# Optimization experiments

Hardware: AMD Instinct MI355X
Metric: run time of the kernel (lower is better)

The kernel has to match this reference:

```python
import jax, jax.numpy as jnp
import numpy as np

B, L, DK, DV, H, DKL, DVL, R = 64, 4096, 128, 128, 4, 64, 128, 128


def setup_inputs() -> dict:
    key = jax.random.key(0)
    ks = jax.random.split(key, 7)
    K = jax.random.normal(ks[0], (B, L, DK), dtype=jnp.float32)
    V = jax.random.normal(ks[1], (B, L, DV), dtype=jnp.float32)
    mask = jax.random.uniform(ks[2], (B, L)) < 0.25
    mask = mask.at[:, 0].set(False)
    # Learned parameters (Wq is zeros at init in the original; use small random
    # values so the softmax is non-degenerate for correctness testing)
    Wq = jax.random.normal(ks[3], (H, DKL), dtype=jnp.float32) * 0.02
    Wk = jax.random.normal(ks[4], (DK, H, DKL), dtype=jnp.float32) / np.sqrt(DK)
    Wv = jax.random.normal(ks[5], (DV, H, DVL), dtype=jnp.float32) / np.sqrt(DV)
    Wo = jax.random.normal(ks[6], (H, DVL, R), dtype=jnp.float32) / np.sqrt(H * DVL)
    return {"K": K, "V": V, "mask": mask, "Wq": Wq, "Wk": Wk, "Wv": Wv, "Wo": Wo}


def reference(K, V, mask, Wq, Wk, Wv, Wo):
    # scale = 1/sqrt(dim_q), dim_q == dim_k
    scale = 1.0 / jnp.sqrt(jnp.asarray(K.shape[-1], K.dtype))
    Kp = jnp.einsum('bld,dhk->blhk', K, Wk)          # (B, L, H, DKL)
    Vp = jnp.einsum('ble,ehv->blhv', V, Wv)          # (B, L, H, DVL)
    QK = jnp.einsum('hk,blhk->blh', Wq, Kp)          # (B, L, H)
    QK = jnp.where(mask[..., None], -jnp.inf, QK)    # mask over set axis L
    w = jax.nn.softmax(scale * QK, axis=-2)          # softmax over L (dim=-2)
    # nanmean over the set axis (masked positions contribute w=0; NaN entries,
    # if present in V, are skipped exactly as torch.nanmean does)
    QKV = jnp.nanmean(w[..., None] * Vp, axis=-3)    # (B, H, DVL)
    return jnp.einsum('bhv,hvr->br', QKV, Wo)        # (B, R)
```

## Files before the change

### kernel.cpp

```cpp
#include <hip/hip_runtime.h>
#include <math.h>

#define BB   64
#define LL   4096
#define DKC  128
#define DVC  128
#define HC   4
#define DKLC 64
#define DVLC 128
#define RC   128

#define NCA  64
#define CA   64

typedef float f4v __attribute__((ext_vector_type(4)));
__device__ __forceinline__ float4 ntload4(const float4* p) {
    f4v v = __builtin_nontemporal_load((const f4v*)p);
    return make_float4(v.x, v.y, v.z, v.w);
}

__global__ __launch_bounds__(512) void k_foldq(const float* __restrict__ Wq,
                                               const float* __restrict__ Wk,
                                               float* __restrict__ q) {
    int t = threadIdx.x;
    int h = t >> 7;
    int d = t & 127;
    float acc = 0.f;
#pragma unroll 8
    for (int k = 0; k < DKLC; ++k)
        acc += Wq[h * DKLC + k] * Wk[(d * HC + h) * DKLC + k];
    q[h * DKC + d] = acc;
}

__global__ __launch_bounds__(256) void k_fused(const float* __restrict__ K,
                                               const float* __restrict__ V,
                                               const int*   __restrict__ mask,
                                               const float* __restrict__ q,
                                               float* __restrict__ stats,
                                               float* __restrict__ partWV) {
    const int bid = blockIdx.x;
    const int b   = bid >> 6;
    const int a   = bid & (NCA - 1);
    const int l0  = a * CA;
    const int t   = threadIdx.x;

    __shared__ float4 partS[CA][17];
    __shared__ float  P4s[CA * HC];
    __shared__ float  redm[4][HC];
    __shared__ float  redz[4][HC];

    {
        const int rg = t >> 4;
        const int i8 = t & 15;
        float4 qf1[HC], qf2[HC];
#pragma unroll
        for (int h = 0; h < HC; ++h) {
            qf1[h] = ((const float4*)q)[h * 32 + i8];
            qf2[h] = ((const float4*)q)[h * 32 + i8 + 16];
        }
        const float4* Kg = (const float4*)(K + ((long)b * LL + l0) * DKC);
#pragma unroll
        for (int it = 0; it < CA / 16; ++it) {
            int r = it * 16 + rg;
            float4 k1 = ntload4(&Kg[r * 32 + i8]);
            float4 k2 = ntload4(&Kg[r * 32 + i8 + 16]);
            float4 d;
            d.x = k1.x*qf1[0].x + k1.y*qf1[0].y + k1.z*qf1[0].z + k1.w*qf1[0].w
                + k2.x*qf2[0].x + k2.y*qf2[0].y + k2.z*qf2[0].z + k2.w*qf2[0].w;
            d.y = k1.x*qf1[1].x + k1.y*qf1[1].y + k1.z*qf1[1].z + k1.w*qf1[1].w
                + k2.x*qf2[1].x + k2.y*qf2[1].y + k2.z*qf2[1].z + k2.w*qf2[1].w;
            d.z = k1.x*qf1[2].x + k1.y*qf1[2].y + k1.z*qf1[2].z + k1.w*qf1[2].w
                + k2.x*qf2[2].x + k2.y*qf2[2].y + k2.z*qf2[2].z + k2.w*qf2[2].w;
            d.w = k1.x*qf1[3].x + k1.y*qf1[3].y + k1.z*qf1[3].z + k1.w*qf1[3].w
                + k2.x*qf2[3].x + k2.y*qf2[3].y + k2.z*qf2[3].z + k2.w*qf2[3].w;
            partS[r][i8] = d;
        }
    }
    __syncthreads();

    {
        const int r2 = t >> 2;
        const int h2 = t & 3;
        float s = 0.f;
#pragma unroll
        for (int c = 0; c < 16; ++c)
            s += ((const float*)partS)[(r2 * 17 + c) * 4 + h2];

        int mk = __builtin_nontemporal_load(mask + (long)b * LL + l0 + r2);
        const float scale = 0.08838834764831844f;
        s = mk ? -INFINITY : s * scale;

        float m = s;
#pragma unroll
        for (int off = 4; off <= 32; off <<= 1)
            m = fmaxf(m, __shfl_xor(m, off));
        if ((t & 63) < 4) redm[t >> 6][h2] = m;
        __syncthreads();
        float mm = fmaxf(fmaxf(redm[0][h2], redm[1][h2]),
                         fmaxf(redm[2][h2], redm[3][h2]));
        float mu = (mm == -INFINITY) ? 0.f : mm;

        float p = expf(s - mu);
        float z = p;
#pragma unroll
        for (int off = 4; off <= 32; off <<= 1)
            z += __shfl_xor(z, off);
        if ((t & 63) < 4) redz[t >> 6][h2] = z;
        P4s[t] = p;
        if (t < HC) stats[(long)bid * 8 + t] = mm;
        __syncthreads();
        if (t < HC)
            stats[(long)bid * 8 + 4 + t] =
                redz[0][t] + redz[1][t] + redz[2][t] + redz[3][t];
    }

    const int rg3 = t >> 5;
    const int i4  = t & 31;
    const int w   = t >> 6;
    float4 acc[HC];
#pragma unroll
    for (int h = 0; h < HC; ++h) acc[h] = make_float4(0.f, 0.f, 0.f, 0.f);

    const float4* Vb = (const float4*)(V + ((long)b * LL + l0) * DVC);
#pragma unroll
    for (int it = 0; it < CA / 8; ++it) {
        int r = it * 8 + rg3;
        float4 vv = ntload4(&Vb[r * 32 + i4]);
        float4 w4 = ((const float4*)P4s)[r];
        acc[0].x += w4.x*vv.x; acc[0].y += w4.x*vv.y; acc[0].z += w4.x*vv.z; acc[0].w += w4.x*vv.w;
        acc[1].x += w4.y*vv.x; acc[1].y += w4.y*vv.y; acc[1].z += w4.y*vv.z; acc[1].w += w4.y*vv.w;
        acc[2].x += w4.z*vv.x; acc[2].y += w4.z*vv.y; acc[2].z += w4.z*vv.z; acc[2].w += w4.z*vv.w;
        acc[3].x += w4.w*vv.x; acc[3].y += w4.w*vv.y; acc[3].z += w4.w*vv.z; acc[3].w += w4.w*vv.w;
    }
#pragma unroll
    for (int h = 0; h < HC; ++h) {
        acc[h].x += __shfl_xor(acc[h].x, 32);
        acc[h].y += __shfl_xor(acc[h].y, 32);
        acc[h].z += __shfl_xor(acc[h].z, 32);
        acc[h].w += __shfl_xor(acc[h].w, 32);
    }
    float4 (*red)[32][HC] = (float4 (*)[32][HC])partS;
    __syncthreads();
    if ((t & 63) < 32) {
#pragma unroll
        for (int h = 0; h < HC; ++h) red[w][i4][h] = acc[h];
    }
    __syncthreads();
    if (t < 128) {
        int h = t >> 5, c = t & 31;
        float4 s0 = red[0][c][h], s1 = red[1][c][h];
        float4 s2 = red[2][c][h], s3 = red[3][c][h];
        float4 o;
        o.x = s0.x + s1.x + s2.x + s3.x;
        o.y = s0.y + s1.y + s2.y + s3.y;
        o.z = s0.z + s1.z + s2.z + s3.z;
        o.w = s0.w + s1.w + s2.w + s3.w;
        ((float4*)partWV)[((long)bid * HC + h) * (DVC / 4) + c] = o;
    }
}

__global__ __launch_bounds__(256) void k_out(const float* __restrict__ stats,
                                             const float* __restrict__ partWV,
                                             const float* __restrict__ Wv,
                                             const float* __restrict__ Wo,
                                             float* __restrict__ out) {
    int b = blockIdx.x;
    int t = threadIdx.x;
    __shared__ float WV[HC][DVC];
    __shared__ float QKV[HC * DVLC];
    __shared__ float sc[NCA][HC];
    __shared__ float zinv[HC];

    {
        int h2 = t >> 6, a = t & 63;
        float ma = stats[((long)b * NCA + a) * 8 + h2];
        float za = stats[((long)b * NCA + a) * 8 + 4 + h2];
        float m = ma;
#pragma unroll
        for (int off = 32; off; off >>= 1) m = fmaxf(m, __shfl_xor(m, off));
        float f  = (ma == -INFINITY) ? 0.f : expf(ma - m);
        sc[a][h2] = f;
        float fz = f * za;
#pragma unroll
        for (int off = 32; off; off >>= 1) fz += __shfl_xor(fz, off);
        if (a == 0) zinv[h2] = 1.0f / fz;
    }
    __syncthreads();

    for (int j = t; j < HC * DVC; j += 256) {
        int h = j >> 7, e = j & 127;
        float acc = 0.f;
#pragma unroll 8
        for (int p = 0; p < NCA; ++p)
            acc += sc[p][h] * partWV[(((long)b * NCA + p) * HC + h) * DVC + e];
        WV[h][e] = acc * zinv[h];
    }
    __syncthreads();

    for (int j = t; j < HC * DVLC; j += 256) {
        int h = j >> 7, vv = j & 127;
        float acc = 0.f;
#pragma unroll 8
        for (int e = 0; e < DVC; ++e)
            acc += WV[h][e] * Wv[(e * HC + h) * DVLC + vv];
        QKV[j] = acc * (1.0f / LL);
    }
    __syncthreads();

    for (int r = t; r < RC; r += 256) {
        float acc = 0.f;
#pragma unroll 8
        for (int i = 0; i < HC * DVLC; ++i)
            acc += QKV[i] * Wo[i * RC + r];
        out[b * RC + r] = acc;
    }
}

extern "C" void kernel_launch(void* const* d_in, const int* in_sizes, int n_in,
                              void* d_out, int out_size, void* d_ws, size_t ws_size,
                              hipStream_t stream) {
    (void)in_sizes; (void)n_in; (void)out_size; (void)ws_size;
    const float* K    = (const float*)d_in[0];
    const float* V    = (const float*)d_in[1];
    const int*   mask = (const int*)  d_in[2];
    const float* Wq   = (const float*)d_in[3];
    const float* Wk   = (const float*)d_in[4];
    const float* Wv   = (const float*)d_in[5];
    const float* Wo   = (const float*)d_in[6];
    float* out = (float*)d_out;

    float* q      = (float*)d_ws;
    float* stats  = q + 512;
    float* partWV = stats + (long)BB * NCA * 8;

    k_foldq<<<1, 512, 0, stream>>>(Wq, Wk, q);
    k_fused<<<BB * NCA, 256, 0, stream>>>(K, V, mask, q, stats, partWV);
    k_out<<<BB, 256, 0, stream>>>(stats, partWV, Wv, Wo, out);
}
```

Baseline: 77.86 us.

## Issue K and V loads upfront and compute softmax per wave with shuffles

Each wave now owns 16 rows and issues all of its K, V and mask loads at the start, so V traffic overlaps the score computation instead of waiting behind two barriers. Dot-product reductions, the max and the sum now use wave shuffles instead of shared-memory partials. Per-wave softmax statistics are combined with an online-softmax rescale after a single barrier. This removes several __syncthreads and LDS round trips, at the cost of more registers held per thread and extra exp work for the rescaling.

```diff
diff --git a/kernel.cpp b/kernel.cpp
--- a/kernel.cpp
+++ b/kernel.cpp
@@ -17,6 +17,9 @@
 __device__ __forceinline__ float4 ntload4(const float4* p) {
     f4v v = __builtin_nontemporal_load((const f4v*)p);
     return make_float4(v.x, v.y, v.z, v.w);
+}
+__device__ __forceinline__ float dot4(float4 a, float4 b) {
+    return a.x * b.x + a.y * b.y + a.z * b.z + a.w * b.w;
 }
 
 __global__ __launch_bounds__(512) void k_foldq(const float* __restrict__ Wq,
@@ -43,95 +46,144 @@
     const int a   = bid & (NCA - 1);
     const int l0  = a * CA;
     const int t   = threadIdx.x;
-
-    __shared__ float4 partS[CA][17];
-    __shared__ float  P4s[CA * HC];
-    __shared__ float  redm[4][HC];
-    __shared__ float  redz[4][HC];
-
-    {
-        const int rg = t >> 4;
-        const int i8 = t & 15;
-        float4 qf1[HC], qf2[HC];
-#pragma unroll
-        for (int h = 0; h < HC; ++h) {
-            qf1[h] = ((const float4*)q)[h * 32 + i8];
-            qf2[h] = ((const float4*)q)[h * 32 + i8 + 16];
+    const int w   = t >> 6;
+    const int ln  = t & 63;
+    const int lin = ln & 15;
+    const int rh  = ln >> 5;
+    const int rowbase = l0 + w * 16;
+
+    const float4* Kb = (const float4*)(K + (long)b * LL * DKC);
+    const float4* Vb = (const float4*)(V + (long)b * LL * DVC);
+
+    float4 k0[4], k1[4];
+#pragma unroll
+    for (int p = 0; p < 4; ++p) {
+        int rp = rowbase + p * 4 + (ln >> 4);
+        k0[p] = ntload4(&Kb[rp * 32 + lin]);
+        k1[p] = ntload4(&Kb[rp * 32 + 16 + lin]);
+    }
+    float4 vv[8];
+#pragma unroll
+    for (int it = 0; it < 8; ++it) {
+        int rv = rowbase + it * 2 + rh;
+        vv[it] = ntload4(&Vb[rv * 32 + (ln & 31)]);
+    }
+    int mk[4];
+#pragma unroll
+    for (int p = 0; p < 4; ++p)
+        mk[p] = __builtin_nontemporal_load(mask + (long)b * LL + rowbase + p * 4 + (ln >> 4));
+
+    float4 qa[HC], qb[HC];
+#pragma unroll
+    for (int h = 0; h < HC; ++h) {
+        qa[h] = ((const float4*)q)[h * 32 + lin];
+        qb[h] = ((const float4*)q)[h * 32 + 16 + lin];
+    }
+
+    const float scale = 0.08838834764831844f;
+    float4 d[4];
+#pragma unroll
+    for (int p = 0; p < 4; ++p) {
+        float4 dd;
+        dd.x = dot4(k0[p], qa[0]) + dot4(k1[p], qb[0]);
+        dd.y = dot4(k0[p], qa[1]) + dot4(k1[p], qb[1]);
+        dd.z = dot4(k0[p], qa[2]) + dot4(k1[p], qb[2]);
+        dd.w = dot4(k0[p], qa[3]) + dot4(k1[p], qb[3]);
+#pragma unroll
+        for (int off = 1; off <= 8; off <<= 1) {
+            dd.x += __shfl_xor(dd.x, off);
+            dd.y += __shfl_xor(dd.y, off);
+            dd.z += __shfl_xor(dd.z, off);
+            dd.w += __shfl_xor(dd.w, off);
         }
-        const float4* Kg = (const float4*)(K + ((long)b * LL + l0) * DKC);
-#pragma unroll
-        for (int it = 0; it < CA / 16; ++it) {
-            int r = it * 16 + rg;
-            float4 k1 = ntload4(&Kg[r * 32 + i8]);
-            float4 k2 = ntload4(&Kg[r * 32 + i8 + 16]);
-            float4 d;
-            d.x = k1.x*qf1[0].x + k1.y*qf1[0].y + k1.z*qf1[0].z + k1.w*qf1[0].w
-                + k2.x*qf2[0].x + k2.y*qf2[0].y + k2.z*qf2[0].z + k2.w*qf2[0].w;
-            d.y = k1.x*qf1[1].x + k1.y*qf1[1].y + k1.z*qf1[1].z + k1.w*qf1[1].w
-                + k2.x*qf2[1].x + k2.y*qf2[1].y + k2.z*qf2[1].z + k2.w*qf2[1].w;
-            d.z = k1.x*qf1[2].x + k1.y*qf1[2].y + k1.z*qf1[2].z + k1.w*qf1[2].w
-                + k2.x*qf2[2].x + k2.y*qf2[2].y + k2.z*qf2[2].z + k2.w*qf2[2].w;
-            d.w = k1.x*qf1[3].x + k1.y*qf1[3].y + k1.z*qf1[3].z + k1.w*qf1[3].w
-                + k2.x*qf2[3].x + k2.y*qf2[3].y + k2.z*qf2[3].z + k2.w*qf2[3].w;
-            partS[r][i8] = d;
-        }
-    }
-    __syncthreads();
-
-    {
-        const int r2 = t >> 2;
-        const int h2 = t & 3;
-        float s = 0.f;
-#pragma unroll
-        for (int c = 0; c < 16; ++c)
-            s += ((const float*)partS)[(r2 * 17 + c) * 4 + h2];
-
-        int mk = __builtin_nontemporal_load(mask + (long)b * LL + l0 + r2);
-        const float scale = 0.08838834764831844f;
-        s = mk ? -INFINITY : s * scale;
-
-        float m = s;
-#pragma unroll
-        for (int off = 4; off <= 32; off <<= 1)
-            m = fmaxf(m, __shfl_xor(m, off));
-        if ((t & 63) < 4) redm[t >> 6][h2] = m;
-        __syncthreads();
-        float mm = fmaxf(fmaxf(redm[0][h2], redm[1][h2]),
-                         fmaxf(redm[2][h2], redm[3][h2]));
-        float mu = (mm == -INFINITY) ? 0.f : mm;
-
-        float p = expf(s - mu);
-        float z = p;
-#pragma unroll
-        for (int off = 4; off <= 32; off <<= 1)
-            z += __shfl_xor(z, off);
-        if ((t & 63) < 4) redz[t >> 6][h2] = z;
-        P4s[t] = p;
-        if (t < HC) stats[(long)bid * 8 + t] = mm;
-        __syncthreads();
-        if (t < HC)
-            stats[(long)bid * 8 + 4 + t] =
-                redz[0][t] + redz[1][t] + redz[2][t] + redz[3][t];
-    }
-
-    const int rg3 = t >> 5;
-    const int i4  = t & 31;
-    const int w   = t >> 6;
+        d[p].x = mk[p] ? -INFINITY : dd.x * scale;
+        d[p].y = mk[p] ? -INFINITY : dd.y * scale;
+        d[p].z = mk[p] ? -INFINITY : dd.z * scale;
+        d[p].w = mk[p] ? -INFINITY : dd.w * scale;
+    }
+
+    float4 m4;
+    m4.x = fmaxf(fmaxf(d[0].x, d[1].x), fmaxf(d[2].x, d[3].x));
+    m4.y = fmaxf(fmaxf(d[0].y, d[1].y), fmaxf(d[2].y, d[3].y));
+    m4.z = fmaxf(fmaxf(d[0].z, d[1].z), fmaxf(d[2].z, d[3].z));
+    m4.w = fmaxf(fmaxf(d[0].w, d[1].w), fmaxf(d[2].w, d[3].w));
+#pragma unroll
+    for (int off = 16; off <= 32; off <<= 1) {
+        m4.x = fmaxf(m4.x, __shfl_xor(m4.x, off));
+        m4.y = fmaxf(m4.y, __shfl_xor(m4.y, off));
+        m4.z = fmaxf(m4.z, __shfl_xor(m4.z, off));
+        m4.w = fmaxf(m4.w, __shfl_xor(m4.w, off));
+    }
+    float4 mu4;
+    mu4.x = (m4.x == -INFINITY) ? 0.f : m4.x;
+    mu4.y = (m4.y == -INFINITY) ? 0.f : m4.y;
+    mu4.z = (m4.z == -INFINITY) ? 0.f : m4.z;
+    mu4.w = (m4.w == -INFINITY) ? 0.f : m4.w;
+
+    float4 pp[4];
+#pragma unroll
+    for (int p = 0; p < 4; ++p) {
+        pp[p].x = expf(d[p].x - mu4.x);
+        pp[p].y = expf(d[p].y - mu4.y);
+        pp[p].z = expf(d[p].z - mu4.z);
+        pp[p].w = expf(d[p].w - mu4.w);
+    }
+    float4 z4;
+    z4.x = pp[0].x + pp[1].x + pp[2].x + pp[3].x;
+    z4.y = pp[0].y + pp[1].y + pp[2].y + pp[3].y;
+    z4.z = pp[0].z + pp[1].z + pp[2].z + pp[3].z;
+    z4.w = pp[0].w + pp[1].w + pp[2].w + pp[3].w;
+#pragma unroll
+    for (int off = 16; off <= 32; off <<= 1) {
+        z4.x += __shfl_xor(z4.x, off);
+        z4.y += __shfl_xor(z4.y, off);
+        z4.z += __shfl_xor(z4.z, off);
+        z4.w += __shfl_xor(z4.w, off);
+    }
+
     float4 acc[HC];
 #pragma unroll
     for (int h = 0; h < HC; ++h) acc[h] = make_float4(0.f, 0.f, 0.f, 0.f);
-
-    const float4* Vb = (const float4*)(V + ((long)b * LL + l0) * DVC);
-#pragma unroll
-    for (int it = 0; it < CA / 8; ++it) {
-        int r = it * 8 + rg3;
-        float4 vv = ntload4(&Vb[r * 32 + i4]);
-        float4 w4 = ((const float4*)P4s)[r];
-        acc[0].x += w4.x*vv.x; acc[0].y += w4.x*vv.y; acc[0].z += w4.x*vv.z; acc[0].w += w4.x*vv.w;
-        acc[1].x += w4.y*vv.x; acc[1].y += w4.y*vv.y; acc[1].z += w4.y*vv.z; acc[1].w += w4.y*vv.w;
-        acc[2].x += w4.z*vv.x; acc[2].y += w4.z*vv.y; acc[2].z += w4.z*vv.z; acc[2].w += w4.z*vv.w;
-        acc[3].x += w4.w*vv.x; acc[3].y += w4.w*vv.y; acc[3].z += w4.w*vv.z; acc[3].w += w4.w*vv.w;
-    }
+#pragma unroll
+    for (int it = 0; it < 8; ++it) {
+        int src = (((2 * it) & 3) + rh) * 16 + lin;
+        float4 w4;
+        w4.x = __shfl(pp[it >> 1].x, src);
+        w4.y = __shfl(pp[it >> 1].y, src);
+        w4.z = __shfl(pp[it >> 1].z, src);
+        w4.w = __shfl(pp[it >> 1].w, src);
+        float4 v = vv[it];
+        acc[0].x += w4.x*v.x; acc[0].y += w4.x*v.y; acc[0].z += w4.x*v.z; acc[0].w += w4.x*v.w;
+        acc[1].x += w4.y*v.x; acc[1].y += w4.y*v.y; acc[1].z += w4.y*v.z; acc[1].w += w4.y*v.w;
+        acc[2].x += w4.z*v.x; acc[2].y += w4.z*v.y; acc[2].z += w4.z*v.z; acc[2].w += w4.z*v.w;
+        acc[3].x += w4.w*v.x; acc[3].y += w4.w*v.y; acc[3].z += w4.w*v.z; acc[3].w += w4.w*v.w;
+    }
+
+    __shared__ float4 wsm[4], wsz[4];
+    __shared__ float4 red[4][32][HC];
+    if (ln == 0) { wsm[w] = m4; wsz[w] = z4; }
+    __syncthreads();
+
+    float4 mb;
+    mb.x = fmaxf(fmaxf(wsm[0].x, wsm[1].x), fmaxf(wsm[2].x, wsm[3].x));
+    mb.y = fmaxf(fmaxf(wsm[0].y, wsm[1].y), fmaxf(wsm[2].y, wsm[3].y));
+    mb.z = fmaxf(fmaxf(wsm[0].z, wsm[1].z), fmaxf(wsm[2].z, wsm[3].z));
+    mb.w = fmaxf(fmaxf(wsm[0].w, wsm[1].w), fmaxf(wsm[2].w, wsm[3].w));
+    float4 mub;
+    mub.x = (mb.x == -INFINITY) ? 0.f : mb.x;
+    mub.y = (mb.y == -INFINITY) ? 0.f : mb.y;
+    mub.z = (mb.z == -INFINITY) ? 0.f : mb.z;
+    mub.w = (mb.w == -INFINITY) ? 0.f : mb.w;
+    float4 fw;
+    fw.x = (wsm[w].x == -INFINITY) ? 0.f : expf(wsm[w].x - mub.x);
+    fw.y = (wsm[w].y == -INFINITY) ? 0.f : expf(wsm[w].y - mub.y);
+    fw.z = (wsm[w].z == -INFINITY) ? 0.f : expf(wsm[w].z - mub.z);
+    fw.w = (wsm[w].w == -INFINITY) ? 0.f : expf(wsm[w].w - mub.w);
+    acc[0].x *= fw.x; acc[0].y *= fw.x; acc[0].z *= fw.x; acc[0].w *= fw.x;
+    acc[1].x *= fw.y; acc[1].y *= fw.y; acc[1].z *= fw.y; acc[1].w *= fw.y;
+    acc[2].x *= fw.z; acc[2].y *= fw.z; acc[2].z *= fw.z; acc[2].w *= fw.z;
+    acc[3].x *= fw.w; acc[3].y *= fw.w; acc[3].z *= fw.w; acc[3].w *= fw.w;
+
 #pragma unroll
     for (int h = 0; h < HC; ++h) {
         acc[h].x += __shfl_xor(acc[h].x, 32);
@@ -139,11 +191,27 @@
         acc[h].z += __shfl_xor(acc[h].z, 32);
         acc[h].w += __shfl_xor(acc[h].w, 32);
     }
-    float4 (*red)[32][HC] = (float4 (*)[32][HC])partS;
-    __syncthreads();
-    if ((t & 63) < 32) {
-#pragma unroll
-        for (int h = 0; h < HC; ++h) red[w][i4][h] = acc[h];
+    if (ln < 32) {
+#pragma unroll
+        for (int h = 0; h < HC; ++h) red[w][ln][h] = acc[h];
+    }
+    if (t == 0) {
+        stats[(long)bid * 8 + 0] = mb.x;
+        stats[(long)bid * 8 + 1] = mb.y;
+        stats[(long)bid * 8 + 2] = mb.z;
+        stats[(long)bid * 8 + 3] = mb.w;
+        float zx = 0.f, zy = 0.f, zz = 0.f, zw = 0.f;
+#pragma unroll
+        for (int w2 = 0; w2 < 4; ++w2) {
+            zx += ((wsm[w2].x == -INFINITY) ? 0.f : expf(wsm[w2].x - mub.x)) * wsz[w2].x;
+            zy += ((wsm[w2].y == -INFINITY) ? 0.f : expf(wsm[w2].y - mub.y)) * wsz[w2].y;
+            zz += ((wsm[w2].z == -INFINITY) ? 0.f : expf(wsm[w2].z - mub.z)) * wsz[w2].z;
+            zw += ((wsm[w2].w == -INFINITY) ? 0.f : expf(wsm[w2].w - mub.w)) * wsz[w2].w;
+        }
+        stats[(long)bid * 8 + 4] = zx;
+        stats[(long)bid * 8 + 5] = zy;
+        stats[(long)bid * 8 + 6] = zz;
+        stats[(long)bid * 8 + 7] = zw;
     }
     __syncthreads();
     if (t < 128) {
```

Measured after the change: 77.76 us (median of 2 runs). No clear change (-0.1%).
